# Optimization experiments

Hardware: AMD Instinct MI355X
Metric: run time of the kernel (lower is better)

Reference implementation:

```python
import jax, jax.numpy as jnp
import numpy as np

N, E, NG, H, BD, L, B = 4000, 50000, 12, 128, 128, 2, 100

def _gelu(x):
    return jax.nn.gelu(x, approximate=False)

def forward(pos, vel, charges, grid0, rand_SO3, batch, edge_index,
            W_basis1, b_basis1, W_basis2, b_basis2,
            W_fbasis1, b_fbasis1, W_fbasis2, b_fbasis2,
            W_embed, W_conv, W_fiber, b_conv, ln_gamma, ln_beta,
            W_ff1, b_ff1, W_ff2, b_ff2, W_ro1, b_ro1, W_ro2, b_ro2):
    n_nodes = pos.shape[0]
    n_graphs = rand_SO3.shape[0]
    n = grid0.shape[0]
    src, dst = edge_index[0], edge_index[1]
    # per-graph randomly rotated S2 grid
    grid_graph = jnp.einsum('bij,nj->bni', rand_SO3, grid0)    # [B,n,3]
    grid_node = grid_graph[batch]                               # [N,n,3]
    grid_edge = grid_node[src]                                  # [E,n,3]
    # R3S2 Euclidean invariants (separable): parallel + perpendicular parts of rel_pos wrt each grid orientation
    rel = pos[src] - pos[dst]                                   # [E,3]
    inv1 = jnp.einsum('ed,end->en', rel, grid_edge)[..., None]  # [E,n,1]
    inv2 = jnp.linalg.norm(rel[:, None, :] - inv1 * grid_edge, axis=-1, keepdims=True)
    cp = (charges[src] * charges[dst])[:, None, :]              # [E,1,1]
    ei = jnp.concatenate([inv1, inv2, jnp.broadcast_to(cp, inv1.shape)], -1)  # [E,n,3]
    # PolynomialFeatures(degree=2): [x, flatten(x outer x)] -> 3+9=12
    ei_poly = jnp.concatenate([ei, (ei[..., :, None] * ei[..., None, :]).reshape(ei.shape[:-1] + (9,))], -1)
    basis = _gelu(_gelu(ei_poly @ W_basis1 + b_basis1) @ W_basis2 + b_basis2)  # [E,n,BD]
    # fiber invariants: pairwise grid dot products (rotation cancels) -> [n,n,1]; poly deg 2 -> [n,n,2]
    fi = jnp.sum(grid0[:, None, :] * grid0[None, :, :], -1, keepdims=True)
    fi_poly = jnp.concatenate([fi, fi * fi], -1)
    fiber_basis = _gelu(_gelu(fi_poly @ W_fbasis1 + b_fbasis1) @ W_fbasis2 + b_fbasis2)  # [n,n,BD]
    # node features projected to sphere
    ones = jnp.ones((n_nodes, 1), pos.dtype)
    cnt = jax.ops.segment_sum(ones, batch, num_segments=n_graphs)
    mean_pos = jax.ops.segment_sum(pos, batch, num_segments=n_graphs) / jnp.maximum(cnt, 1.0)
    rel_pos = pos - mean_pos[batch]
    v_sph = jnp.einsum('nd,nkd->nk', vel, grid_node)[..., None]
    p_sph = jnp.einsum('nd,nkd->nk', rel_pos, grid_node)[..., None]
    c_sph = jnp.broadcast_to(charges[:, None, :], (n_nodes, n, 1))
    vn = jnp.linalg.norm(vel, axis=-1, keepdims=True)
    vn_sph = jnp.broadcast_to(vn[:, None, :], (n_nodes, n, 1))
    x = jnp.concatenate([v_sph, p_sph, c_sph, vn_sph], -1) @ W_embed  # [N,n,H]
    # SeparableBundleConvNext stack
    for l in range(W_conv.shape[0]):
        kern = basis @ W_conv[l]                                       # [E,n,H]
        x1 = jax.ops.segment_sum(x[src] * kern, dst, num_segments=n_nodes)  # depthwise spatial conv + scatter-add
        fk = fiber_basis @ W_fiber[l]                                  # [n,n,H]
        x2 = jnp.einsum('boc,poc->bpc', x1, fk) / n + b_conv[l]        # depthwise fiber conv
        mu = jnp.mean(x2, -1, keepdims=True)
        var = jnp.mean((x2 - mu) ** 2, -1, keepdims=True)
        h = (x2 - mu) / jnp.sqrt(var + 1e-5) * ln_gamma[l] + ln_beta[l]
        h = _gelu(h @ W_ff1[l] + b_ff1[l]) @ W_ff2[l] + b_ff2[l]
        x = x + h
    y = _gelu(x @ W_ro1 + b_ro1) @ W_ro2 + b_ro2                       # [N,n,1]
    return jnp.mean(grid_node * y, axis=-2)                            # sphere2vec -> [N,3]

def setup_inputs():
    key = jax.random.key(0)
    ks = jax.random.split(key, 24)
    f = jnp.float32
    # deterministic uniform-ish S2 grid (fibonacci sphere)
    i = np.arange(NG) + 0.5
    phi = np.arccos(1.0 - 2.0 * i / NG)
    th = np.pi * (1.0 + 5.0 ** 0.5) * i
    grid0 = jnp.asarray(np.stack([np.sin(phi) * np.cos(th), np.sin(phi) * np.sin(th), np.cos(phi)], -1), f)
    # random SO(3) per graph via unit quaternions
    q = jax.random.normal(ks[0], (B, 4), f)
    q = q / jnp.linalg.norm(q, axis=-1, keepdims=True)
    w, xq, yq, zq = q[:, 0], q[:, 1], q[:, 2], q[:, 3]
    R = jnp.stack([
        jnp.stack([1 - 2 * (yq ** 2 + zq ** 2), 2 * (xq * yq - zq * w), 2 * (xq * zq + yq * w)], -1),
        jnp.stack([2 * (xq * yq + zq * w), 1 - 2 * (xq ** 2 + zq ** 2), 2 * (yq * zq - xq * w)], -1),
        jnp.stack([2 * (xq * zq - yq * w), 2 * (yq * zq + xq * w), 1 - 2 * (xq ** 2 + yq ** 2)], -1)], -2)
    s = 0.05
    return dict(
        pos=jax.random.normal(ks[1], (N, 3), f),
        vel=jax.random.normal(ks[2], (N, 3), f),
        charges=jax.random.normal(ks[3], (N, 1), f),
        batch=jnp.sort(jax.random.randint(ks[4], (N,), 0, B)),
        edge_index=jax.random.randint(ks[5], (2, E), 0, N),
        grid0=grid0, rand_SO3=R,
        W_basis1=jax.random.normal(ks[6], (12, H), f) * s, b_basis1=jnp.zeros((H,), f),
        W_basis2=jax.random.normal(ks[7], (H, BD), f) * s, b_basis2=jnp.zeros((BD,), f),
        W_fbasis1=jax.random.normal(ks[8], (2, H), f) * s, b_fbasis1=jnp.zeros((H,), f),
        W_fbasis2=jax.random.normal(ks[9], (H, BD), f) * s, b_fbasis2=jnp.zeros((BD,), f),
        W_embed=jax.random.normal(ks[10], (4, H), f) * s,
        W_conv=jax.random.normal(ks[11], (L, BD, H), f) * s,
        W_fiber=jax.random.normal(ks[12], (L, BD, H), f) * s,
        b_conv=jnp.zeros((L, H), f),
        ln_gamma=jnp.ones((L, H), f), ln_beta=jnp.zeros((L, H), f),
        W_ff1=jax.random.normal(ks[13], (L, H, 4 * H), f) * s, b_ff1=jnp.zeros((L, 4 * H), f),
        W_ff2=jax.random.normal(ks[14], (L, 4 * H, H), f) * s, b_ff2=jnp.zeros((L, H), f),
        W_ro1=jax.random.normal(ks[15], (H, H), f) * s, b_ro1=jnp.zeros((H,), f),
        W_ro2=jax.random.normal(ks[16], (H, 1), f) * s, b_ro2=jnp.zeros((1,), f),
    )

def reference(pos, vel, charges, batch, edge_index, grid0, rand_SO3,
              W_basis1, b_basis1, W_basis2, b_basis2,
              W_fbasis1, b_fbasis1, W_fbasis2, b_fbasis2,
              W_embed, W_conv, W_fiber, b_conv, ln_gamma, ln_beta,
              W_ff1, b_ff1, W_ff2, b_ff2, W_ro1, b_ro1, W_ro2, b_ro2):
    return forward(pos, vel, charges, grid0, rand_SO3, batch, edge_index,
                   W_basis1, b_basis1, W_basis2, b_basis2,
                   W_fbasis1, b_fbasis1, W_fbasis2, b_fbasis2,
                   W_embed, W_conv, W_fiber, b_conv, ln_gamma, ln_beta,
                   W_ff1, b_ff1, W_ff2, b_ff2, W_ro1, b_ro1, W_ro2, b_ro2)
```

## Files before the change

kernel.cpp:

```cpp
#include <hip/hip_runtime.h>

typedef unsigned short u16;
typedef short s16x8 __attribute__((ext_vector_type(8)));
typedef float f32x4 __attribute__((ext_vector_type(4)));

constexpr int NNODES = 4000;
constexpr int NEDGES = 50000;
constexpr int NGRID  = 12;
constexpr int HD     = 128;
constexpr int H4     = 512;
constexpr int NLAY   = 2;

constexpr size_t OFF_GN   = 0;
constexpr size_t OFF_PS   = 144000;
constexpr size_t OFF_CNT  = 144304;
constexpr size_t OFF_FK   = 144512;
constexpr size_t OFF_X    = 181376;
constexpr size_t OFF_X1   = 6325376;
constexpr size_t OFF_WB   = 12469376;
constexpr size_t OFF_ROWP = 12625024;
constexpr size_t OFF_DEG  = 12629032;
constexpr size_t OFF_CUR  = 12633032;
constexpr size_t OFF_ESRT = 12637032;
constexpr size_t OFF_EIPB = 12687032;
constexpr size_t OFF_W1T  = 17487416;
constexpr size_t OFF_SRCS = 17489464;
constexpr size_t OFF_END_SLOW = 17539464;
constexpr size_t OFF_BAS  = 17539464;
constexpr size_t KERN_F   = 38400000;
constexpr size_t OFF_END_FAST  = OFF_BAS + KERN_F;
constexpr size_t OFF_END_DUAL  = OFF_BAS + 2*KERN_F;

constexpr size_t WB_W2T = 0;
constexpr size_t WB_WCT = 16384;
constexpr size_t WB_F1T = 49152;
constexpr size_t WB_F2T = 180224;

__device__ __forceinline__ u16 f2bf(float f){
  union { float f; unsigned int i; } v; v.f = f;
  unsigned int x = v.i;
  x += 0x7fffu + ((x >> 16) & 1u);
  return (u16)(x >> 16);
}
__device__ __forceinline__ float bf2f(u16 u){
  union { unsigned int i; float f; } v; v.i = ((unsigned int)u) << 16; return v.f;
}
__device__ __forceinline__ float gelu_f(float x){
  return 0.5f * x * (1.0f + erff(x * 0.70710678118654752f));
}
__device__ __forceinline__ float waveReduceSum(float v){
  #pragma unroll
  for(int off = 32; off > 0; off >>= 1) v += __shfl_xor(v, off, 64);
  return v;
}
__device__ __forceinline__ f32x4 mfma16(s16x8 a, s16x8 b, f32x4 c){
  return __builtin_amdgcn_mfma_f32_16x16x32_bf16(a, b, c, 0, 0, 0);
}

__global__ void k_stats(const float* __restrict__ pos, const int* __restrict__ batch,
                        float* __restrict__ possum, float* __restrict__ pcnt){
  int n = blockIdx.x * 256 + threadIdx.x;
  if(n >= NNODES) return;
  int b = batch[n];
  atomicAdd(&possum[b*3+0], pos[n*3+0]);
  atomicAdd(&possum[b*3+1], pos[n*3+1]);
  atomicAdd(&possum[b*3+2], pos[n*3+2]);
  atomicAdd(&pcnt[b], 1.0f);
}

__global__ void k_gridnode(const float* __restrict__ g0, const float* __restrict__ R,
                           const int* __restrict__ batch, float* __restrict__ grid_node){
  int idx = blockIdx.x * 256 + threadIdx.x;
  if(idx >= NNODES*NGRID) return;
  int n = idx / NGRID, k = idx % NGRID;
  int b = batch[n];
  float g[3];
  #pragma unroll
  for(int j=0;j<3;j++) g[j] = g0[k*3+j];
  #pragma unroll
  for(int i=0;i<3;i++){
    float s = 0.f;
    #pragma unroll
    for(int j=0;j<3;j++) s += R[b*9+i*3+j] * g[j];
    grid_node[idx*3+i] = s;
  }
}

__global__ __launch_bounds__(128) void k_embed(
    const float* __restrict__ pos, const float* __restrict__ vel, const float* __restrict__ charges,
    const int* __restrict__ batch, const float* __restrict__ possum, const float* __restrict__ pcnt,
    const float* __restrict__ grid_node, const float* __restrict__ W_embed, float* __restrict__ x)
{
  int n = blockIdx.x; int t = threadIdx.x;
  __shared__ float feats[NGRID][4];
  __shared__ float sgn[NGRID][3];
  if(t < 36) sgn[t/3][t%3] = grid_node[n*36 + t];
  __syncthreads();
  if(t < NGRID){
    int b = batch[n];
    float inv = 1.0f / fmaxf(pcnt[b], 1.0f);
    float v0=vel[n*3], v1=vel[n*3+1], v2=vel[n*3+2];
    float p0=pos[n*3]   - possum[b*3]*inv;
    float p1=pos[n*3+1] - possum[b*3+1]*inv;
    float p2=pos[n*3+2] - possum[b*3+2]*inv;
    float g0=sgn[t][0], g1=sgn[t][1], g2=sgn[t][2];
    feats[t][0] = v0*g0 + v1*g1 + v2*g2;
    feats[t][1] = p0*g0 + p1*g1 + p2*g2;
    feats[t][2] = charges[n];
    feats[t][3] = sqrtf(v0*v0 + v1*v1 + v2*v2);
  }
  __syncthreads();
  float w0=W_embed[0*HD+t], w1=W_embed[1*HD+t];
  float w2=W_embed[2*HD+t], w3=W_embed[3*HD+t];
  #pragma unroll
  for(int k=0;k<NGRID;k++)
    x[(n*NGRID+k)*HD + t] = feats[k][0]*w0 + feats[k][1]*w1 + feats[k][2]*w2 + feats[k][3]*w3;
}

__global__ __launch_bounds__(128) void k_fiber(
    const float* __restrict__ g0, const float* __restrict__ Wf1, const float* __restrict__ bfb1,
    const float* __restrict__ Wf2, const float* __restrict__ bfb2, const float* __restrict__ W_fiber,
    float* __restrict__ fk)
{
  int po = blockIdx.x; int p = po / NGRID, o = po % NGRID; int c = threadIdx.x;
  __shared__ float st[HD];
  __shared__ float sfb[HD];
  float fi = 0.f;
  #pragma unroll
  for(int j=0;j<3;j++) fi += g0[p*3+j] * g0[o*3+j];
  float f2 = fi*fi;
  st[c] = gelu_f(fi*Wf1[c] + f2*Wf1[HD+c] + bfb1[c]);
  __syncthreads();
  float a = bfb2[c];
  for(int j=0;j<HD;j++) a += st[j] * Wf2[j*HD+c];
  sfb[c] = gelu_f(a);
  __syncthreads();
  for(int l=0;l<NLAY;l++){
    float s = 0.f;
    for(int j=0;j<HD;j++) s += sfb[j] * W_fiber[l*HD*HD + j*HD + c];
    fk[(l*144 + po)*HD + c] = s;
  }
}

__global__ void k_prep(const float* __restrict__ W_b2, const float* __restrict__ W_b1,
                       const float* __restrict__ W_conv, const float* __restrict__ W_ff1,
                       const float* __restrict__ W_ff2,
                       u16* __restrict__ W2T, u16* __restrict__ W1T, u16* __restrict__ WCT,
                       u16* __restrict__ F1T, u16* __restrict__ F2T){
  int idx = blockIdx.x * 256 + threadIdx.x;
  if(idx < 16384){
    int r = idx >> 7, c = idx & 127;
    W2T[c*128 + r] = f2bf(W_b2[idx]);
    return;
  }
  idx -= 16384;
  if(idx < 4096){
    int c = idx >> 5, f = idx & 31;
    W1T[idx] = (f < 12) ? f2bf(W_b1[f*HD + c]) : (u16)0;
    return;
  }
  idx -= 4096;
  if(idx < 32768){
    int l = idx >> 14, j = idx & 16383;
    int r = j >> 7, c = j & 127;
    WCT[l*16384 + c*128 + r] = f2bf(W_conv[l*16384 + j]);
    return;
  }
  idx -= 32768;
  if(idx < 131072){
    int l = idx >> 16, j = idx & 65535;
    int r = j / 512, c = j % 512;
    F1T[l*65536 + c*128 + r] = f2bf(W_ff1[l*65536 + j]);
    return;
  }
  idx -= 131072;
  if(idx < 131072){
    int l = idx >> 16, j = idx & 65535;
    int r = j / 128, c = j % 128;
    F2T[l*65536 + c*512 + r] = f2bf(W_ff2[l*65536 + j]);
  }
}

__global__ void k_prepro(const float* __restrict__ W_ro1, u16* __restrict__ RO1T){
  int idx = blockIdx.x * 256 + threadIdx.x;
  if(idx >= 16384) return;
  int r = idx >> 7, c = idx & 127;
  RO1T[c*128 + r] = f2bf(W_ro1[idx]);
}

__global__ void k_deg(const int* __restrict__ eidx, int* __restrict__ deg){
  int e = blockIdx.x * 256 + threadIdx.x;
  if(e >= NEDGES) return;
  atomicAdd(&deg[eidx[NEDGES + e]], 1);
}

__global__ __launch_bounds__(256) void k_scan(const int* __restrict__ deg, int* __restrict__ rowptr){
  int t = threadIdx.x;
  __shared__ int part[256];
  int base = t * 16;
  int lp[16]; int s = 0;
  #pragma unroll
  for(int i=0;i<16;i++){
    int idx = base + i;
    int v = (idx < NNODES) ? deg[idx] : 0;
    lp[i] = s; s += v;
  }
  part[t] = s;
  __syncthreads();
  for(int off=1; off<256; off<<=1){
    int v2 = (t >= off) ? part[t-off] : 0;
    __syncthreads();
    part[t] += v2;
    __syncthreads();
  }
  int excl = part[t] - s;
  #pragma unroll
  for(int i=0;i<16;i++){
    int idx = base + i;
    if(idx < NNODES) rowptr[idx] = excl + lp[i];
  }
  if(t == 255) rowptr[NNODES] = part[255];
}

__global__ void k_bucket(const int* __restrict__ eidx, const int* __restrict__ rowptr,
                         int* __restrict__ cur, int* __restrict__ esorted, int* __restrict__ srcs){
  int e = blockIdx.x * 256 + threadIdx.x;
  if(e >= NEDGES) return;
  int d = eidx[NEDGES + e];
  int p = atomicAdd(&cur[d], 1);
  int slot = rowptr[d] + p;
  esorted[slot] = e;
  srcs[slot] = eidx[e];
}

__global__ void k_einv(const int* __restrict__ esorted, const int* __restrict__ eidx,
                       const float* __restrict__ pos, const float* __restrict__ charges,
                       const float* __restrict__ grid_node, u16* __restrict__ eipb){
  int row = blockIdx.x * 256 + threadIdx.x;
  if(row >= NEDGES*NGRID) return;
  int p = row / NGRID, kg = row - p*NGRID;
  int e = esorted[p];
  int sr = eidx[e], ds = eidx[NEDGES + e];
  float r0 = pos[sr*3]   - pos[ds*3];
  float r1 = pos[sr*3+1] - pos[ds*3+1];
  float r2 = pos[sr*3+2] - pos[ds*3+2];
  float cp = charges[sr] * charges[ds];
  float g0 = grid_node[sr*36 + kg*3];
  float g1 = grid_node[sr*36 + kg*3 + 1];
  float g2 = grid_node[sr*36 + kg*3 + 2];
  float inv1 = r0*g0 + r1*g1 + r2*g2;
  float d0 = r0 - inv1*g0, d1 = r1 - inv1*g1, d2 = r2 - inv1*g2;
  float inv2 = sqrtf(d0*d0 + d1*d1 + d2*d2);
  float ei[3] = {inv1, inv2, cp};
  s16x8 lo, hi;
  #pragma unroll
  for(int i=0;i<3;i++) lo[i] = (short)f2bf(ei[i]);
  lo[3] = (short)f2bf(ei[0]*ei[0]);
  lo[4] = (short)f2bf(ei[0]*ei[1]);
  lo[5] = (short)f2bf(ei[0]*ei[2]);
  lo[6] = (short)f2bf(ei[1]*ei[0]);
  lo[7] = (short)f2bf(ei[1]*ei[1]);
  hi[0] = (short)f2bf(ei[1]*ei[2]);
  hi[1] = (short)f2bf(ei[2]*ei[0]);
  hi[2] = (short)f2bf(ei[2]*ei[1]);
  hi[3] = (short)f2bf(ei[2]*ei[2]);
  hi[4] = 0; hi[5] = 0; hi[6] = 0; hi[7] = 0;
  *(s16x8*)&eipb[(size_t)row*16]     = lo;
  *(s16x8*)&eipb[(size_t)row*16 + 8] = hi;
}

constexpr int T1S = 136;

__global__ __launch_bounds__(256) void k_kern(
    const u16* __restrict__ eipb, const u16* __restrict__ W1T,
    const float* __restrict__ b1, const float* __restrict__ b2,
    const u16* __restrict__ W2T, const u16* __restrict__ WCT,
    u16* __restrict__ kern, int nl, size_t kstride)
{
  int t = threadIdx.x;
  int lane = t & 63, w = t >> 6, quad = lane >> 4, l16 = lane & 15;
  size_t R0 = (size_t)blockIdx.x * 64;
  __shared__ __align__(16) u16 s_buf[64*T1S];

  float b1v[2], b2v[2];
  #pragma unroll
  for(int nt=0;nt<2;nt++){
    b1v[nt] = b1[(2*w+nt)*16 + l16];
    b2v[nt] = b2[(2*w+nt)*16 + l16];
  }
  const s16x8 zvec = {0,0,0,0,0,0,0,0};

  {
    f32x4 a1[4][2];
    #pragma unroll
    for(int mt=0;mt<4;mt++)
      #pragma unroll
      for(int nt=0;nt<2;nt++) a1[mt][nt] = (f32x4){0.f,0.f,0.f,0.f};
    s16x8 Af[4];
    #pragma unroll
    for(int mt=0;mt<4;mt++){
      s16x8 v = *(const s16x8*)&eipb[(R0 + mt*16 + l16)*16 + (quad&1)*8];
      if(quad >= 2) v = zvec;
      Af[mt] = v;
    }
    #pragma unroll
    for(int nt=0;nt<2;nt++){
      s16x8 Bf = *(const s16x8*)&W1T[((2*w+nt)*16 + l16)*32 + quad*8];
      #pragma unroll
      for(int mt=0;mt<4;mt++) a1[mt][nt] = mfma16(Af[mt], Bf, a1[mt][nt]);
    }
    #pragma unroll
    for(int mt=0;mt<4;mt++)
      #pragma unroll
      for(int nt=0;nt<2;nt++)
        #pragma unroll
        for(int i=0;i<4;i++)
          s_buf[(mt*16 + quad*4 + i)*T1S + (2*w+nt)*16 + l16] = f2bf(gelu_f(a1[mt][nt][i] + b1v[nt]));
  }
  __syncthreads();
  f32x4 a2[4][2];
  #pragma unroll
  for(int mt=0;mt<4;mt++)
    #pragma unroll
    for(int nt=0;nt<2;nt++) a2[mt][nt] = (f32x4){0.f,0.f,0.f,0.f};
  #pragma unroll
  for(int ks=0; ks<4; ks++){
    s16x8 Af[4];
    #pragma unroll
    for(int mt=0;mt<4;mt++)
      Af[mt] = *(const s16x8*)&s_buf[(mt*16 + l16)*T1S + ks*32 + quad*8];
    #pragma unroll
    for(int nt=0;nt<2;nt++){
      s16x8 Bf = *(const s16x8*)&W2T[((2*w+nt)*16 + l16)*HD + ks*32 + quad*8];
      #pragma unroll
      for(int mt=0;mt<4;mt++) a2[mt][nt] = mfma16(Af[mt], Bf, a2[mt][nt]);
    }
  }
  __syncthreads();
  #pragma unroll
  for(int mt=0;mt<4;mt++)
    #pragma unroll
    for(int nt=0;nt<2;nt++)
      #pragma unroll
      for(int i=0;i<4;i++)
        s_buf[(mt*16 + quad*4 + i)*T1S + (2*w+nt)*16 + l16] = f2bf(gelu_f(a2[mt][nt][i] + b2v[nt]));
  __syncthreads();
  for(int l=0; l<nl; l++){
    f32x4 a3[4][2];
    #pragma unroll
    for(int mt=0;mt<4;mt++)
      #pragma unroll
      for(int nt=0;nt<2;nt++) a3[mt][nt] = (f32x4){0.f,0.f,0.f,0.f};
    #pragma unroll
    for(int ks=0; ks<4; ks++){
      s16x8 Af[4];
      #pragma unroll
      for(int mt=0;mt<4;mt++)
        Af[mt] = *(const s16x8*)&s_buf[(mt*16 + l16)*T1S + ks*32 + quad*8];
      #pragma unroll
      for(int nt=0;nt<2;nt++){
        s16x8 Bf = *(const s16x8*)&WCT[l*16384 + ((2*w+nt)*16 + l16)*HD + ks*32 + quad*8];
        #pragma unroll
        for(int mt=0;mt<4;mt++) a3[mt][nt] = mfma16(Af[mt], Bf, a3[mt][nt]);
      }
    }
    #pragma unroll
    for(int mt=0;mt<4;mt++)
      #pragma unroll
      for(int nt=0;nt<2;nt++)
        #pragma unroll
        for(int i=0;i<4;i++)
          kern[l*kstride + (R0 + mt*16 + quad*4 + i)*HD + (2*w+nt)*16 + l16] = f2bf(a3[mt][nt][i]);
  }
}

__global__ __launch_bounds__(256) void k_gather(
    const u16* __restrict__ kern, const float* __restrict__ x,
    const int* __restrict__ rowptr, const int* __restrict__ srcs,
    const float* __restrict__ fkl, const float* __restrict__ bconv,
    const float* __restrict__ gamma, const float* __restrict__ beta,
    u16* __restrict__ hout)
{
  int n = blockIdx.x, t = threadIdx.x;
  int c = t & 127, half = t >> 7;
  int w = t >> 6, lane = t & 63;
  __shared__ float raw[NGRID*HD];
  __shared__ float red[4][6], red2[4][6];
  int base = rowptr[n];
  int d = rowptr[n+1] - base;
  float acc[6] = {0.f,0.f,0.f,0.f,0.f,0.f};
  int srcn = (d > 0) ? srcs[base] : 0;
  for(int e=0; e<d; e++){
    int nsrc = (e+1 < d) ? srcs[base+e+1] : 0;
    const u16*   kp = &kern[((size_t)(base+e)*NGRID + half*6)*HD + c];
    const float* xp = &x[((size_t)srcn*NGRID + half*6)*HD + c];
    #pragma unroll
    for(int kk=0;kk<6;kk++)
      acc[kk] += bf2f(kp[kk*HD]) * xp[kk*HD];
    srcn = nsrc;
  }
  #pragma unroll
  for(int kk=0;kk<6;kk++)
    raw[(half*6+kk)*HD + c] = acc[kk];
  __syncthreads();
  float bc = bconv[c];
  float v[6];
  #pragma unroll
  for(int kk=0;kk<6;kk++){
    int p = half*6 + kk;
    float a = 0.f;
    #pragma unroll
    for(int o=0;o<NGRID;o++)
      a += raw[o*HD + c] * fkl[(p*NGRID+o)*HD + c];
    v[kk] = a * (1.0f/12.0f) + bc;
  }
  #pragma unroll
  for(int kk=0;kk<6;kk++){
    float s = waveReduceSum(v[kk]);
    if(lane == 0) red[w][kk] = s;
  }
  __syncthreads();
  float dd[6];
  #pragma unroll
  for(int kk=0;kk<6;kk++){
    float mu = (red[half*2][kk] + red[half*2+1][kk]) * (1.0f/128.0f);
    dd[kk] = v[kk] - mu;
    float s2 = waveReduceSum(dd[kk]*dd[kk]);
    if(lane == 0) red2[w][kk] = s2;
  }
  __syncthreads();
  float ga = gamma[c], be = beta[c];
  #pragma unroll
  for(int kk=0;kk<6;kk++){
    float var = (red2[half*2][kk] + red2[half*2+1][kk]) * (1.0f/128.0f);
    float inv = 1.0f / sqrtf(var + 1e-5f);
    hout[((size_t)n*NGRID + half*6 + kk)*HD + c] = f2bf(dd[kk] * inv * ga + be);
  }
}

constexpr int STS = 520;
__global__ __launch_bounds__(256) void k_ff(
    const u16* __restrict__ F1T, const float* __restrict__ bf1,
    const u16* __restrict__ F2T, const float* __restrict__ bf2,
    const u16* __restrict__ hin, float* __restrict__ x)
{
  int t = threadIdx.x;
  int n0 = blockIdx.x * 2;
  __shared__ __align__(16) u16 sxh[32*T1S];
  __shared__ __align__(16) u16 st[32*STS];

  for(int i=t; i<2*NGRID*HD; i+=256){
    int nd = i / (NGRID*HD), rem = i - nd*NGRID*HD;
    int r = rem >> 7, cc = rem & 127;
    sxh[(nd*16 + r)*T1S + cc] = hin[(size_t)n0*NGRID*HD + i];
  }
  for(int i=t; i<4*T1S; i+=256){ sxh[12*T1S + i] = 0; sxh[28*T1S + i] = 0; }
  __syncthreads();
  {
    int lane = t & 63, w = t >> 6, quad = lane >> 4, l16 = lane & 15;
    f32x4 acc1[2][8];
    #pragma unroll
    for(int mt=0;mt<2;mt++)
      #pragma unroll
      for(int j=0;j<8;j++) acc1[mt][j] = (f32x4){0.f,0.f,0.f,0.f};
    #pragma unroll
    for(int ks=0; ks<4; ks++){
      s16x8 Af0 = *(const s16x8*)&sxh[l16*T1S + ks*32 + quad*8];
      s16x8 Af1 = *(const s16x8*)&sxh[(16 + l16)*T1S + ks*32 + quad*8];
      #pragma unroll
      for(int j=0;j<8;j++){
        int nt = w*8 + j;
        s16x8 Bf = *(const s16x8*)&F1T[((size_t)(nt*16 + l16))*HD + ks*32 + quad*8];
        acc1[0][j] = mfma16(Af0, Bf, acc1[0][j]);
        acc1[1][j] = mfma16(Af1, Bf, acc1[1][j]);
      }
    }
    #pragma unroll
    for(int j=0;j<8;j++){
      int col = (w*8+j)*16 + l16;
      float bv = bf1[col];
      #pragma unroll
      for(int mt=0;mt<2;mt++)
        #pragma unroll
        for(int i=0;i<4;i++){
          int row = mt*16 + quad*4 + i;
          st[row*STS + col] = f2bf(gelu_f(acc1[mt][j][i] + bv));
        }
    }
  }
  __syncthreads();
  {
    int lane = t & 63, w = t >> 6, quad = lane >> 4, l16 = lane & 15;
    f32x4 acc2[2][2];
    #pragma unroll
    for(int mt=0;mt<2;mt++)
      #pragma unroll
      for(int j=0;j<2;j++) acc2[mt][j] = (f32x4){0.f,0.f,0.f,0.f};
    for(int ks=0; ks<16; ks++){
      s16x8 Af0 = *(const s16x8*)&st[l16*STS + ks*32 + quad*8];
      s16x8 Af1 = *(const s16x8*)&st[(16 + l16)*STS + ks*32 + quad*8];
      #pragma unroll
      for(int j=0;j<2;j++){
        int nt = w*2 + j;
        s16x8 Bf = *(const s16x8*)&F2T[((size_t)(nt*16 + l16))*H4 + ks*32 + quad*8];
        acc2[0][j] = mfma16(Af0, Bf, acc2[0][j]);
        acc2[1][j] = mfma16(Af1, Bf, acc2[1][j]);
      }
    }
    #pragma unroll
    for(int j=0;j<2;j++){
      int col = (w*2+j)*16 + l16;
      float bv = bf2[col];
      #pragma unroll
      for(int mt=0;mt<2;mt++)
        #pragma unroll
        for(int i=0;i<4;i++){
          int row = quad*4 + i;
          if(row < NGRID){
            size_t idx = ((size_t)(n0+mt)*NGRID + row)*HD + col;
            x[idx] += acc2[mt][j][i] + bv;
          }
        }
    }
  }
}

__global__ __launch_bounds__(256) void k_conv_slow(
    const u16* __restrict__ eipb, const u16* __restrict__ W1T,
    const float* __restrict__ b1, const float* __restrict__ b2,
    const u16* __restrict__ W2T, const u16* __restrict__ WCT,
    const float* __restrict__ x,
    const int* __restrict__ rowptr, const int* __restrict__ srcs,
    float* __restrict__ x1o)
{
  int n = blockIdx.x; int t = threadIdx.x;
  int lane = t & 63, w = t >> 6, quad = lane >> 4, l16 = lane & 15;

  __shared__ __align__(16) u16 s_t1h[48*T1S];
  __shared__ __align__(16) u16 s_bas[48*T1S];
  __shared__ __align__(16) float accLDS[NGRID*HD];

  int base = rowptr[n];
  int d = rowptr[n+1] - base;

  float b1v[2], b2v[2];
  #pragma unroll
  for(int nt=0;nt<2;nt++){
    b1v[nt] = b1[(2*w+nt)*16 + l16];
    b2v[nt] = b2[(2*w+nt)*16 + l16];
  }

  for(int i=t; i<NGRID*HD; i+=256) accLDS[i] = 0.f;
  __syncthreads();

  f32x4 accv[3][2];
  #pragma unroll
  for(int mt=0;mt<3;mt++)
    #pragma unroll
    for(int nt=0;nt<2;nt++) accv[mt][nt] = (f32x4){0.f,0.f,0.f,0.f};

  const s16x8 zvec = {0,0,0,0,0,0,0,0};

  for(int ch=0; ch<d; ch+=4){
    size_t rowb = (size_t)(base + ch) * NGRID;
    s16x8 Af1[3];
    #pragma unroll
    for(int mt=0;mt<3;mt++){
      s16x8 v = *(const s16x8*)&eipb[(rowb + mt*16 + l16)*16 + (quad&1)*8];
      if(quad >= 2) v = zvec;
      Af1[mt] = v;
    }
    float xv[3][4][2];
    #pragma unroll
    for(int mt=0;mt<3;mt++)
      #pragma unroll
      for(int i=0;i<4;i++){
        int row = mt*16 + quad*4 + i;
        int e = row / 12;
        int k = row - e*12;
        int ei2 = base + ch + e;
        int srcn = srcs[min(ei2, NEDGES-1)];
        float m = (ch + e < d) ? 1.0f : 0.0f;
        const float* xp = &x[((size_t)srcn*NGRID + k)*HD + l16];
        #pragma unroll
        for(int nt=0;nt<2;nt++)
          xv[mt][i][nt] = xp[(2*w+nt)*16] * m;
      }
    {
      f32x4 a1[3][2];
      #pragma unroll
      for(int mt=0;mt<3;mt++)
        #pragma unroll
        for(int nt=0;nt<2;nt++) a1[mt][nt] = (f32x4){0.f,0.f,0.f,0.f};
      #pragma unroll
      for(int nt=0;nt<2;nt++){
        s16x8 Bf = *(const s16x8*)&W1T[((2*w+nt)*16 + l16)*32 + quad*8];
        #pragma unroll
        for(int mt=0;mt<3;mt++) a1[mt][nt] = mfma16(Af1[mt], Bf, a1[mt][nt]);
      }
      #pragma unroll
      for(int mt=0;mt<3;mt++)
        #pragma unroll
        for(int nt=0;nt<2;nt++)
          #pragma unroll
          for(int i=0;i<4;i++)
            s_t1h[(mt*16 + quad*4 + i)*T1S + (2*w+nt)*16 + l16] = f2bf(gelu_f(a1[mt][nt][i] + b1v[nt]));
    }
    __syncthreads();
    {
      f32x4 a2[3][2];
      #pragma unroll
      for(int mt=0;mt<3;mt++)
        #pragma unroll
        for(int nt=0;nt<2;nt++) a2[mt][nt] = (f32x4){0.f,0.f,0.f,0.f};
      #pragma unroll
      for(int ks=0; ks<4; ks++){
        s16x8 Af[3];
        #pragma unroll
        for(int mt=0;mt<3;mt++)
          Af[mt] = *(const s16x8*)&s_t1h[(mt*16 + l16)*T1S + ks*32 + quad*8];
        #pragma unroll
        for(int nt=0;nt<2;nt++){
          s16x8 Bf = *(const s16x8*)&W2T[((2*w+nt)*16 + l16)*HD + ks*32 + quad*8];
          #pragma unroll
          for(int mt=0;mt<3;mt++) a2[mt][nt] = mfma16(Af[mt], Bf, a2[mt][nt]);
        }
      }
      #pragma unroll
      for(int mt=0;mt<3;mt++)
        #pragma unroll
        for(int nt=0;nt<2;nt++)
          #pragma unroll
          for(int i=0;i<4;i++)
            s_bas[(mt*16 + quad*4 + i)*T1S + (2*w+nt)*16 + l16] = f2bf(gelu_f(a2[mt][nt][i] + b2v[nt]));
    }
    __syncthreads();
    {
      f32x4 a3[3][2];
      #pragma unroll
      for(int mt=0;mt<3;mt++)
        #pragma unroll
        for(int nt=0;nt<2;nt++) a3[mt][nt] = (f32x4){0.f,0.f,0.f,0.f};
      #pragma unroll
      for(int ks=0; ks<4; ks++){
        s16x8 Af[3];
        #pragma unroll
        for(int mt=0;mt<3;mt++)
          Af[mt] = *(const s16x8*)&s_bas[(mt*16 + l16)*T1S + ks*32 + quad*8];
        #pragma unroll
        for(int nt=0;nt<2;nt++){
          s16x8 Bf = *(const s16x8*)&WCT[((2*w+nt)*16 + l16)*HD + ks*32 + quad*8];
          #pragma unroll
          for(int mt=0;mt<3;mt++) a3[mt][nt] = mfma16(Af[mt], Bf, a3[mt][nt]);
        }
      }
      #pragma unroll
      for(int mt=0;mt<3;mt++)
        #pragma unroll
        for(int nt=0;nt<2;nt++)
          #pragma unroll
          for(int i=0;i<4;i++)
            accv[mt][nt][i] += a3[mt][nt][i] * xv[mt][i][nt];
    }
  }
  __syncthreads();
  #pragma unroll
  for(int mt=0;mt<3;mt++)
    #pragma unroll
    for(int nt=0;nt<2;nt++)
      #pragma unroll
      for(int i=0;i<4;i++){
        int row = mt*16 + quad*4 + i;
        int k = row % 12;
        atomicAdd(&accLDS[k*HD + (2*w+nt)*16 + l16], accv[mt][nt][i]);
      }
  __syncthreads();
  for(int i=t; i<NGRID*HD; i+=256)
    x1o[(size_t)n*NGRID*HD + i] = accLDS[i];
}

__global__ __launch_bounds__(256) void k_ffln(
    const u16* __restrict__ F1T, const float* __restrict__ bf1,
    const u16* __restrict__ F2T, const float* __restrict__ bf2,
    const float* __restrict__ x1raw,
    const float* __restrict__ fkl, const float* __restrict__ bconv,
    const float* __restrict__ gamma, const float* __restrict__ beta,
    float* __restrict__ x)
{
  int n = blockIdx.x; int t = threadIdx.x;
  int lane = t & 63, w = t >> 6, quad = lane >> 4, l16 = lane & 15;
  __shared__ __align__(16) float raw[NGRID*HD];
  __shared__ __align__(16) u16 sxh[16*T1S];
  __shared__ __align__(16) u16 st[16*STS];

  for(int i=t; i<NGRID*HD; i+=256) raw[i] = x1raw[(size_t)n*NGRID*HD + i];
  for(int i=t; i<4*T1S; i+=256) sxh[12*T1S + i] = 0;
  __syncthreads();

  {
    int c0 = lane, c1 = lane + 64;
    float bc0 = bconv[c0], bc1 = bconv[c1];
    float ga0 = gamma[c0], ga1 = gamma[c1];
    float be0 = beta[c0],  be1 = beta[c1];
    #pragma unroll
    for(int pp=0; pp<3; pp++){
      int p = w + pp*4;
      float a0 = 0.f, a1 = 0.f;
      #pragma unroll
      for(int o=0;o<NGRID;o++){
        a0 += raw[o*HD + c0] * fkl[(p*NGRID+o)*HD + c0];
        a1 += raw[o*HD + c1] * fkl[(p*NGRID+o)*HD + c1];
      }
      float v0 = a0 * (1.0f/12.0f) + bc0;
      float v1 = a1 * (1.0f/12.0f) + bc1;
      float mu = waveReduceSum(v0 + v1) * (1.0f/128.0f);
      float d0 = v0 - mu, d1 = v1 - mu;
      float var = waveReduceSum(d0*d0 + d1*d1) * (1.0f/128.0f);
      float inv = 1.0f / sqrtf(var + 1e-5f);
      sxh[p*T1S + c0] = f2bf(d0 * inv * ga0 + be0);
      sxh[p*T1S + c1] = f2bf(d1 * inv * ga1 + be1);
    }
  }
  __syncthreads();
  {
    f32x4 acc1[8];
    #pragma unroll
    for(int j=0;j<8;j++) acc1[j] = (f32x4){0.f,0.f,0.f,0.f};
    #pragma unroll
    for(int ks=0; ks<4; ks++){
      s16x8 Af = *(const s16x8*)&sxh[l16*T1S + ks*32 + quad*8];
      #pragma unroll
      for(int j=0;j<8;j++){
        int nt = w*8 + j;
        s16x8 Bf = *(const s16x8*)&F1T[((size_t)(nt*16 + l16))*HD + ks*32 + quad*8];
        acc1[j] = mfma16(Af, Bf, acc1[j]);
      }
    }
    #pragma unroll
    for(int j=0;j<8;j++){
      int col = (w*8+j)*16 + l16;
      float bv = bf1[col];
      #pragma unroll
      for(int i=0;i<4;i++){
        int row = quad*4 + i;
        st[row*STS + col] = f2bf(gelu_f(acc1[j][i] + bv));
      }
    }
  }
  __syncthreads();
  {
    f32x4 acc2[2];
    #pragma unroll
    for(int j=0;j<2;j++) acc2[j] = (f32x4){0.f,0.f,0.f,0.f};
    for(int ks=0; ks<16; ks++){
      s16x8 Af = *(const s16x8*)&st[l16*STS + ks*32 + quad*8];
      #pragma unroll
      for(int j=0;j<2;j++){
        int nt = w*2 + j;
        s16x8 Bf = *(const s16x8*)&F2T[((size_t)(nt*16 + l16))*H4 + ks*32 + quad*8];
        acc2[j] = mfma16(Af, Bf, acc2[j]);
      }
    }
    #pragma unroll
    for(int j=0;j<2;j++){
      int col = (w*2+j)*16 + l16;
      float bv = bf2[col];
      #pragma unroll
      for(int i=0;i<4;i++){
        int row = quad*4 + i;
        if(row < NGRID){
          size_t idx = ((size_t)n*NGRID + row)*HD + col;
          x[idx] += acc2[j][i] + bv;
        }
      }
    }
  }
}

__global__ __launch_bounds__(256) void k_readout(
    const float* __restrict__ x, const float* __restrict__ grid_node,
    const u16* __restrict__ RO1T, const float* __restrict__ br1,
    const float* __restrict__ Wr2, const float* __restrict__ br2,
    float* __restrict__ out)
{
  int t = threadIdx.x;
  int n0 = blockIdx.x * 2;
  int lane = t & 63, w = t >> 6, quad = lane >> 4, l16 = lane & 15;
  __shared__ __align__(16) u16 sxh[32*T1S];
  __shared__ float sy[32];
  if(t < 32) sy[t] = 0.f;
  for(int i=t; i<2*NGRID*HD; i+=256){
    int nd = i / (NGRID*HD), rem = i - nd*NGRID*HD;
    int r = rem >> 7, c = rem & 127;
    sxh[(nd*16 + r)*T1S + c] = f2bf(x[(size_t)n0*NGRID*HD + i]);
  }
  for(int i=t; i<4*T1S; i+=256){ sxh[12*T1S + i] = 0; sxh[28*T1S + i] = 0; }
  __syncthreads();
  f32x4 acc[2][2];
  #pragma unroll
  for(int mt=0;mt<2;mt++)
    #pragma unroll
    for(int j=0;j<2;j++) acc[mt][j] = (f32x4){0.f,0.f,0.f,0.f};
  #pragma unroll
  for(int ks=0; ks<4; ks++){
    s16x8 Af0 = *(const s16x8*)&sxh[l16*T1S + ks*32 + quad*8];
    s16x8 Af1 = *(const s16x8*)&sxh[(16 + l16)*T1S + ks*32 + quad*8];
    #pragma unroll
    for(int j=0;j<2;j++){
      int nt = w*2 + j;
      s16x8 Bf = *(const s16x8*)&RO1T[((size_t)(nt*16 + l16))*HD + ks*32 + quad*8];
      acc[0][j] = mfma16(Af0, Bf, acc[0][j]);
      acc[1][j] = mfma16(Af1, Bf, acc[1][j]);
    }
  }
  #pragma unroll
  for(int j=0;j<2;j++){
    int col = (w*2+j)*16 + l16;
    float bv = br1[col];
    float w2v = Wr2[col];
    #pragma unroll
    for(int mt=0;mt<2;mt++)
      #pragma unroll
      for(int i=0;i<4;i++){
        int row = quad*4 + i;
        if(row < NGRID)
          atomicAdd(&sy[mt*16 + row], gelu_f(acc[mt][j][i] + bv) * w2v);
      }
  }
  __syncthreads();
  if(t < 6){
    int nd = t / 3, d = t - nd*3;
    float b2v = br2[0];
    float s = 0.f;
    #pragma unroll
    for(int k=0;k<NGRID;k++)
      s += grid_node[((size_t)(n0+nd)*NGRID + k)*3 + d] * (sy[nd*16 + k] + b2v);
    out[(n0+nd)*3 + d] = s * (1.0f/12.0f);
  }
}

extern "C" void kernel_launch(void* const* d_in, const int* in_sizes, int n_in,
                              void* d_out, int out_size, void* d_ws, size_t ws_size,
                              hipStream_t stream)
{
  const float* pos      = (const float*)d_in[0];
  const float* vel      = (const float*)d_in[1];
  const float* charges  = (const float*)d_in[2];
  const int*   batch    = (const int*)d_in[3];
  const int*   eidx     = (const int*)d_in[4];
  const float* grid0    = (const float*)d_in[5];
  const float* R        = (const float*)d_in[6];
  const float* W_b1     = (const float*)d_in[7];
  const float* b_b1     = (const float*)d_in[8];
  const float* W_b2     = (const float*)d_in[9];
  const float* b_b2     = (const float*)d_in[10];
  const float* W_fb1    = (const float*)d_in[11];
  const float* b_fb1    = (const float*)d_in[12];
  const float* W_fb2    = (const float*)d_in[13];
  const float* b_fb2    = (const float*)d_in[14];
  const float* W_embed  = (const float*)d_in[15];
  const float* W_conv   = (const float*)d_in[16];
  const float* W_fiber  = (const float*)d_in[17];
  const float* b_conv   = (const float*)d_in[18];
  const float* ln_g     = (const float*)d_in[19];
  const float* ln_b     = (const float*)d_in[20];
  const float* W_ff1    = (const float*)d_in[21];
  const float* b_ff1    = (const float*)d_in[22];
  const float* W_ff2    = (const float*)d_in[23];
  const float* b_ff2    = (const float*)d_in[24];
  const float* W_ro1    = (const float*)d_in[25];
  const float* b_ro1    = (const float*)d_in[26];
  const float* W_ro2    = (const float*)d_in[27];
  const float* b_ro2    = (const float*)d_in[28];

  float* ws        = (float*)d_ws;
  float* grid_node = ws + OFF_GN;
  float* possum    = ws + OFF_PS;
  float* pcnt      = ws + OFF_CNT;
  float* fk        = ws + OFF_FK;
  float* x         = ws + OFF_X;
  float* x1        = ws + OFF_X1;
  u16*   WB        = (u16*)(ws + OFF_WB);
  u16*   W2T       = WB + WB_W2T;
  u16*   WCT       = WB + WB_WCT;
  u16*   F1T       = WB + WB_F1T;
  u16*   F2T       = WB + WB_F2T;
  int*   rowptr    = (int*)(ws + OFF_ROWP);
  int*   deg       = (int*)(ws + OFF_DEG);
  int*   cur       = (int*)(ws + OFF_CUR);
  int*   esorted   = (int*)(ws + OFF_ESRT);
  u16*   eipb      = (u16*)(ws + OFF_EIPB);
  u16*   W1T       = (u16*)(ws + OFF_W1T);
  int*   srcs      = (int*)(ws + OFF_SRCS);
  u16*   kern1     = (u16*)(ws + OFF_BAS);
  u16*   RO1T      = (u16*)(ws + OFF_ESRT);
  u16*   hbuf      = (u16*)x1;
  const size_t KSTR = (size_t)600000 * HD;

  const bool fast = (ws_size >= OFF_END_FAST * sizeof(float));
  const bool dual = (ws_size >= OFF_END_DUAL * sizeof(float));

  hipMemsetAsync(possum, 0, 512*sizeof(float), stream);
  hipMemsetAsync(deg, 0, NNODES*sizeof(int), stream);
  hipMemsetAsync(cur, 0, NNODES*sizeof(int), stream);
  hipMemsetAsync(eipb + (size_t)NEDGES*NGRID*16, 0, 48*16*sizeof(u16), stream);

  k_stats<<<(NNODES+255)/256, 256, 0, stream>>>(pos, batch, possum, pcnt);
  k_gridnode<<<(NNODES*NGRID+255)/256, 256, 0, stream>>>(grid0, R, batch, grid_node);
  k_embed<<<NNODES, 128, 0, stream>>>(pos, vel, charges, batch, possum, pcnt, grid_node, W_embed, x);
  k_fiber<<<144, 128, 0, stream>>>(grid0, W_fb1, b_fb1, W_fb2, b_fb2, W_fiber, fk);

  k_prep<<<(315392+255)/256, 256, 0, stream>>>(W_b2, W_b1, W_conv, W_ff1, W_ff2,
                                               W2T, W1T, WCT, F1T, F2T);

  k_deg<<<(NEDGES+255)/256, 256, 0, stream>>>(eidx, deg);
  k_scan<<<1, 256, 0, stream>>>(deg, rowptr);
  k_bucket<<<(NEDGES+255)/256, 256, 0, stream>>>(eidx, rowptr, cur, esorted, srcs);

  k_einv<<<(NEDGES*NGRID+255)/256, 256, 0, stream>>>(esorted, eidx, pos, charges, grid_node, eipb);
  k_prepro<<<64, 256, 0, stream>>>(W_ro1, RO1T);

  if(fast){
    if(dual)
      k_kern<<<9375, 256, 0, stream>>>(eipb, W1T, b_b1, b_b2, W2T, WCT, kern1, 2, KSTR);
    for(int l=0; l<NLAY; l++){
      if(!dual)
        k_kern<<<9375, 256, 0, stream>>>(eipb, W1T, b_b1, b_b2, W2T, WCT + (size_t)l*16384,
                                         kern1, 1, 0);
      const u16* kl = dual ? (kern1 + (size_t)l*KSTR) : kern1;
      k_gather<<<NNODES, 256, 0, stream>>>(kl, x, rowptr, srcs,
          fk + (size_t)l*144*HD, b_conv + l*HD, ln_g + l*HD, ln_b + l*HD, hbuf);
      k_ff<<<NNODES/2, 256, 0, stream>>>(F1T + (size_t)l*65536, b_ff1 + l*H4,
          F2T + (size_t)l*65536, b_ff2 + l*HD, hbuf, x);
    }
  } else {
    for(int l=0; l<NLAY; l++){
      k_conv_slow<<<NNODES, 256, 0, stream>>>(eipb, W1T, b_b1, b_b2, W2T, WCT + (size_t)l*16384,
          x, rowptr, srcs, x1);
      k_ffln<<<NNODES, 256, 0, stream>>>(F1T + (size_t)l*65536, b_ff1 + l*H4,
          F2T + (size_t)l*65536, b_ff2 + l*HD, x1,
          fk + (size_t)l*144*HD, b_conv + l*HD, ln_g + l*HD, ln_b + l*HD, x);
    }
  }

  k_readout<<<NNODES/2, 256, 0, stream>>>(x, grid_node, RO1T, b_ro1, W_ro2, b_ro2, (float*)d_out);
}
```

Measured before the change: 827.2 us.

## Split feed-forward into two dense GEMM kernels and use fast erf approximation

The fused per-node-pair FF kernel, which padded 12 grid rows up to 16 and wasted a quarter of the MFMA work, is split into two kernels over densely packed 32-row tiles. The 512-wide hidden activation goes through global memory, reusing the per-layer kernel buffer that is no longer needed after the gather. GELU now uses an Abramowitz-Stegun polynomial erf approximation with __expf in place of erff. The split adds a global round trip for the hidden activations, and the erf approximation adds small numerical error (around 1e-7 absolute).

```diff
diff --git a/kernel.cpp b/kernel.cpp
--- a/kernel.cpp
+++ b/kernel.cpp
@@ -46,7 +46,12 @@
   union { unsigned int i; float f; } v; v.i = ((unsigned int)u) << 16; return v.f;
 }
 __device__ __forceinline__ float gelu_f(float x){
-  return 0.5f * x * (1.0f + erff(x * 0.70710678118654752f));
+  float z = fabsf(x) * 0.70710678118654752f;
+  float t = 1.0f / (1.0f + 0.3275911f * z);
+  float p = t*(0.254829592f + t*(-0.284496736f + t*(1.421413741f + t*(-1.453152027f + t*1.061405429f))));
+  float erfc_z = p * __expf(-z*z);
+  float phi = (x >= 0.0f) ? (1.0f - 0.5f*erfc_z) : (0.5f*erfc_z);
+  return x * phi;
 }
 __device__ __forceinline__ float waveReduceSum(float v){
   #pragma unroll
@@ -438,90 +443,84 @@
   }
 }
 
-constexpr int STS = 520;
-__global__ __launch_bounds__(256) void k_ff(
+__global__ __launch_bounds__(256) void k_ff1(
     const u16* __restrict__ F1T, const float* __restrict__ bf1,
-    const u16* __restrict__ F2T, const float* __restrict__ bf2,
-    const u16* __restrict__ hin, float* __restrict__ x)
+    const u16* __restrict__ hin, u16* __restrict__ h4)
 {
   int t = threadIdx.x;
-  int n0 = blockIdx.x * 2;
+  size_t r0 = (size_t)blockIdx.x * 32;
+  int lane = t & 63, w = t >> 6, quad = lane >> 4, l16 = lane & 15;
   __shared__ __align__(16) u16 sxh[32*T1S];
-  __shared__ __align__(16) u16 st[32*STS];
-
-  for(int i=t; i<2*NGRID*HD; i+=256){
-    int nd = i / (NGRID*HD), rem = i - nd*NGRID*HD;
-    int r = rem >> 7, cc = rem & 127;
-    sxh[(nd*16 + r)*T1S + cc] = hin[(size_t)n0*NGRID*HD + i];
-  }
-  for(int i=t; i<4*T1S; i+=256){ sxh[12*T1S + i] = 0; sxh[28*T1S + i] = 0; }
-  __syncthreads();
-  {
-    int lane = t & 63, w = t >> 6, quad = lane >> 4, l16 = lane & 15;
-    f32x4 acc1[2][8];
+  for(int i=t; i<32*HD/8; i+=256){
+    int r = (i*8) >> 7, cc = (i*8) & 127;
+    *(s16x8*)&sxh[r*T1S + cc] = *(const s16x8*)&hin[r0*HD + (size_t)i*8];
+  }
+  __syncthreads();
+  f32x4 acc[2][8];
+  #pragma unroll
+  for(int mt=0;mt<2;mt++)
+    #pragma unroll
+    for(int j=0;j<8;j++) acc[mt][j] = (f32x4){0.f,0.f,0.f,0.f};
+  #pragma unroll
+  for(int ks=0; ks<4; ks++){
+    s16x8 Af0 = *(const s16x8*)&sxh[l16*T1S + ks*32 + quad*8];
+    s16x8 Af1 = *(const s16x8*)&sxh[(16 + l16)*T1S + ks*32 + quad*8];
+    #pragma unroll
+    for(int j=0;j<8;j++){
+      int nt = w*8 + j;
+      s16x8 Bf = *(const s16x8*)&F1T[((size_t)(nt*16 + l16))*HD + ks*32 + quad*8];
+      acc[0][j] = mfma16(Af0, Bf, acc[0][j]);
+      acc[1][j] = mfma16(Af1, Bf, acc[1][j]);
+    }
+  }
+  #pragma unroll
+  for(int j=0;j<8;j++){
+    int col = (w*8+j)*16 + l16;
+    float bv = bf1[col];
     #pragma unroll
     for(int mt=0;mt<2;mt++)
       #pragma unroll
-      for(int j=0;j<8;j++) acc1[mt][j] = (f32x4){0.f,0.f,0.f,0.f};
-    #pragma unroll
-    for(int ks=0; ks<4; ks++){
-      s16x8 Af0 = *(const s16x8*)&sxh[l16*T1S + ks*32 + quad*8];
-      s16x8 Af1 = *(const s16x8*)&sxh[(16 + l16)*T1S + ks*32 + quad*8];
-      #pragma unroll
-      for(int j=0;j<8;j++){
-        int nt = w*8 + j;
-        s16x8 Bf = *(const s16x8*)&F1T[((size_t)(nt*16 + l16))*HD + ks*32 + quad*8];
-        acc1[0][j] = mfma16(Af0, Bf, acc1[0][j]);
-        acc1[1][j] = mfma16(Af1, Bf, acc1[1][j]);
-      }
-    }
-    #pragma unroll
-    for(int j=0;j<8;j++){
-      int col = (w*8+j)*16 + l16;
-      float bv = bf1[col];
-      #pragma unroll
-      for(int mt=0;mt<2;mt++)
-        #pragma unroll
-        for(int i=0;i<4;i++){
-          int row = mt*16 + quad*4 + i;
-          st[row*STS + col] = f2bf(gelu_f(acc1[mt][j][i] + bv));
-        }
-    }
-  }
-  __syncthreads();
-  {
-    int lane = t & 63, w = t >> 6, quad = lane >> 4, l16 = lane & 15;
-    f32x4 acc2[2][2];
+      for(int i=0;i<4;i++){
+        int row = mt*16 + quad*4 + i;
+        h4[(r0 + row)*H4 + col] = f2bf(gelu_f(acc[mt][j][i] + bv));
+      }
+  }
+}
+
+__global__ __launch_bounds__(256) void k_ff2(
+    const u16* __restrict__ F2T, const float* __restrict__ bf2,
+    const u16* __restrict__ h4, float* __restrict__ x)
+{
+  int t = threadIdx.x;
+  size_t r0 = (size_t)blockIdx.x * 32;
+  int lane = t & 63, w = t >> 6, quad = lane >> 4, l16 = lane & 15;
+  f32x4 acc[2][2];
+  #pragma unroll
+  for(int mt=0;mt<2;mt++)
+    #pragma unroll
+    for(int j=0;j<2;j++) acc[mt][j] = (f32x4){0.f,0.f,0.f,0.f};
+  for(int ks=0; ks<16; ks++){
+    s16x8 Af0 = *(const s16x8*)&h4[(r0 + l16)*H4 + ks*32 + quad*8];
+    s16x8 Af1 = *(const s16x8*)&h4[(r0 + 16 + l16)*H4 + ks*32 + quad*8];
+    #pragma unroll
+    for(int j=0;j<2;j++){
+      int nt = w*2 + j;
+      s16x8 Bf = *(const s16x8*)&F2T[((size_t)(nt*16 + l16))*H4 + ks*32 + quad*8];
+      acc[0][j] = mfma16(Af0, Bf, acc[0][j]);
+      acc[1][j] = mfma16(Af1, Bf, acc[1][j]);
+    }
+  }
+  #pragma unroll
+  for(int j=0;j<2;j++){
+    int col = (w*2+j)*16 + l16;
+    float bv = bf2[col];
     #pragma unroll
     for(int mt=0;mt<2;mt++)
       #pragma unroll
-      for(int j=0;j<2;j++) acc2[mt][j] = (f32x4){0.f,0.f,0.f,0.f};
-    for(int ks=0; ks<16; ks++){
-      s16x8 Af0 = *(const s16x8*)&st[l16*STS + ks*32 + quad*8];
-      s16x8 Af1 = *(const s16x8*)&st[(16 + l16)*STS + ks*32 + quad*8];
-      #pragma unroll
-      for(int j=0;j<2;j++){
-        int nt = w*2 + j;
-        s16x8 Bf = *(const s16x8*)&F2T[((size_t)(nt*16 + l16))*H4 + ks*32 + quad*8];
-        acc2[0][j] = mfma16(Af0, Bf, acc2[0][j]);
-        acc2[1][j] = mfma16(Af1, Bf, acc2[1][j]);
-      }
-    }
-    #pragma unroll
-    for(int j=0;j<2;j++){
-      int col = (w*2+j)*16 + l16;
-      float bv = bf2[col];
-      #pragma unroll
-      for(int mt=0;mt<2;mt++)
-        #pragma unroll
-        for(int i=0;i<4;i++){
-          int row = quad*4 + i;
-          if(row < NGRID){
-            size_t idx = ((size_t)(n0+mt)*NGRID + row)*HD + col;
-            x[idx] += acc2[mt][j][i] + bv;
-          }
-        }
-    }
+      for(int i=0;i<4;i++){
+        size_t row = r0 + mt*16 + quad*4 + i;
+        x[row*HD + col] += acc[mt][j][i] + bv;
+      }
   }
 }
 
@@ -679,6 +678,7 @@
     x1o[(size_t)n*NGRID*HD + i] = accLDS[i];
 }
 
+constexpr int STS = 520;
 __global__ __launch_bounds__(256) void k_ffln(
     const u16* __restrict__ F1T, const float* __restrict__ bf1,
     const u16* __restrict__ F2T, const float* __restrict__ bf2,
@@ -928,10 +928,11 @@
         k_kern<<<9375, 256, 0, stream>>>(eipb, W1T, b_b1, b_b2, W2T, WCT + (size_t)l*16384,
                                          kern1, 1, 0);
       const u16* kl = dual ? (kern1 + (size_t)l*KSTR) : kern1;
+      u16* h4 = dual ? (kern1 + (size_t)l*KSTR) : kern1;
       k_gather<<<NNODES, 256, 0, stream>>>(kl, x, rowptr, srcs,
           fk + (size_t)l*144*HD, b_conv + l*HD, ln_g + l*HD, ln_b + l*HD, hbuf);
-      k_ff<<<NNODES/2, 256, 0, stream>>>(F1T + (size_t)l*65536, b_ff1 + l*H4,
-          F2T + (size_t)l*65536, b_ff2 + l*HD, hbuf, x);
+      k_ff1<<<NNODES*NGRID/32, 256, 0, stream>>>(F1T + (size_t)l*65536, b_ff1 + l*H4, hbuf, h4);
+      k_ff2<<<NNODES*NGRID/32, 256, 0, stream>>>(F2T + (size_t)l*65536, b_ff2 + l*HD, h4, x);
     }
   } else {
     for(int l=0; l<NLAY; l++){
```

New measurement: 820.5 us. No clear change (-0.8%).
